# Performance work log

Measured on AMD Instinct MI355X. Metric: run time of the kernel, lower is better.

The kernel has to match this reference:

```python
import jax, jax.numpy as jnp
import numpy as np
from jax import lax

B, L = 16384, 32
HID, CIN = 8, 2
N_SUB = 2            # RK4 substeps per spline interval (fixed-step stand-in for torchcde's adaptive solver)
T10_LO, T10_HI = 0.1, 7.0


def push_zeros(a):
    # torch: move nonzero entries of each row to the right end, zeros to the left.
    # stable ascending sort on validity key (0 for zeros, 1 for valid) reproduces this exactly
    # because the invalid entries are exactly 0.
    keys = (a != 0).astype(jnp.int32)
    order = jnp.argsort(keys, axis=1)  # jax sorts are stable
    return jnp.take_along_axis(a, order, axis=1)


def setup_inputs() -> dict:
    key = jax.random.key(0)
    ks = jax.random.split(key, 12)
    fa_len = jax.random.randint(ks[0], (B, 1), L // 2, L + 1)          # 16..32 valid points
    valid = jnp.arange(L)[None, :] < fa_len                             # (B, L)
    X_fa_in = jnp.where(valid, jax.random.uniform(ks[1], (B, L), minval=0.1, maxval=1.1), 0.0)
    fa_vals_in = jnp.where(valid, jax.random.uniform(ks[2], (B, L), minval=0.05, maxval=0.45), 0.0)
    TR_vals = jax.random.uniform(ks[3], (B, 1), minval=0.003, maxval=0.01)
    fa_mask = valid

    def lin(k, fout, fin):
        kw, kb = jax.random.split(k)
        s = 1.0 / np.sqrt(fin)
        return (jax.random.uniform(kw, (fout, fin), minval=-s, maxval=s),
                jax.random.uniform(kb, (fout,), minval=-s, maxval=s))

    W_init, b_init = lin(ks[4], HID, CIN)        # self.initial: Linear(2, 8)
    W1, b1 = lin(ks[5], 256, HID)                # CDE_Func.linear1
    W2, b2 = lin(ks[6], CIN * HID, 256)          # CDE_Func.linear2
    Wr1, br1 = lin(ks[7], 200, HID)              # reg_T10
    Wr2, br2 = lin(ks[8], 200, 200)
    Wr3, br3 = lin(ks[9], 1, 200)
    return dict(X_fa_in=X_fa_in, fa_vals_in=fa_vals_in, TR_vals=TR_vals,
                W_init=W_init, b_init=b_init, W1=W1, b1=b1, W2=W2, b2=b2,
                Wr1=Wr1, br1=br1, Wr2=Wr2, br2=br2, Wr3=Wr3, br3=br3,
                fa_mask=fa_mask, fa_len=fa_len)


def _forward(X_fa_in, fa_vals_in, TR_vals, W_init, b_init, W1, b1, W2, b2,
             Wr1, br1, Wr2, br2, Wr3, br3, fa_mask, fa_len):
    fl = fa_len[:, 0]                       # (B,) int
    fl_f = fl.astype(X_fa_in.dtype)
    mean = jnp.sum(X_fa_in, axis=1) / fl_f
    Xn = X_fa_in / mean[:, None]
    X_fa = push_zeros(Xn)
    fa_vals = push_zeros(fa_vals_in)
    bidx = jnp.arange(X_fa.shape[0])
    last_X = X_fa[bidx, fl - 1][:, None]            # pushed array indexed at fa_len-1 (as in torch)
    last_fa = fa_vals_in[bidx, fl - 1][:, None]     # original array indexed at fa_len-1
    X_fa = jnp.where(X_fa == 0.0, last_X, X_fa)
    fa_vals = jnp.where(fa_vals == 0.0, last_fa, fa_vals)
    x = jnp.stack([fa_vals, X_fa], axis=-1)         # (B, L, 2): channels (fa, X)

    # Hermite cubic with backward differences, unit knot spacing t_i = i
    diffs = x[:, 1:] - x[:, :-1]                    # (B, L-1, C)
    m = jnp.concatenate([diffs[:, :1], diffs], axis=1)  # m_0 = fwd diff, m_i = backward diff
    X0s, X1s = x[:, :-1], x[:, 1:]                  # per-interval knot values (B, L-1, C)
    M0s, M1s = m[:, :-1], m[:, 1:]

    z0 = x[:, 0] @ W_init.T + b_init                # X.evaluate(interval[0]) == first knot

    def f(z):  # CDE vector field: (B, HID) -> (B, HID, CIN)
        h = jax.nn.relu(z @ W1.T + b1)
        g = jnp.tanh(h @ W2.T + b2)
        return g.reshape(z.shape[0], HID, CIN)

    hstep = 1.0 / N_SUB
    nI = x.shape[1] - 1
    intervals = jnp.repeat(jnp.arange(nI), N_SUB)
    s0s = jnp.tile(jnp.arange(N_SUB) * hstep, nI).astype(x.dtype)

    def step(z, ts):
        i, s0 = ts
        x0, x1 = X0s[:, i], X1s[:, i]
        m0, m1 = M0s[:, i], M1s[:, i]

        def dX(s):  # spline derivative dX/dt at local coord s in [0,1]
            s2 = s * s
            return ((6 * s2 - 6 * s) * x0 + (3 * s2 - 4 * s + 1) * m0 +
                    (-6 * s2 + 6 * s) * x1 + (3 * s2 - 2 * s) * m1)

        def F(s, zz):
            return jnp.einsum('bhc,bc->bh', f(zz), dX(s))

        k1 = F(s0, z)
        k2 = F(s0 + hstep / 2, z + 0.5 * hstep * k1)
        k3 = F(s0 + hstep / 2, z + 0.5 * hstep * k2)
        k4 = F(s0 + hstep, z + hstep * k3)
        return z + (hstep / 6) * (k1 + 2 * k2 + 2 * k3 + k4), None

    z_T, _ = lax.scan(step, z0, (intervals, s0s))

    h1 = jax.nn.gelu(z_T @ Wr1.T + br1, approximate=False)
    h2 = jax.nn.gelu(h1 @ Wr2.T + br2, approximate=False)
    t = (h2 @ Wr3.T + br3)[:, 0]
    T10 = T10_LO + jax.nn.sigmoid(t)[:, None] * (T10_HI - T10_LO)   # (B, 1)
    R1 = 1.0 / T10
    E = jnp.exp(-TR_vals * R1)                                      # (B, 1)
    X_out = (1 - E) * jnp.sin(fa_vals_in) / (1 - jnp.cos(fa_vals_in) * E)
    mean2 = jnp.sum(X_out, axis=1) / fl_f
    X_out = X_out / mean2[:, None]
    M0 = jnp.ones_like(T10)
    return X_out, T10, M0


def reference(X_fa_in, fa_vals_in, TR_vals, W_init, b_init, W1, b1, W2, b2,
              Wr1, br1, Wr2, br2, Wr3, br3, fa_mask, fa_len):
    return _forward(X_fa_in, fa_vals_in, TR_vals, W_init, b_init, W1, b1, W2, b2,
                    Wr1, br1, Wr2, br2, Wr3, br3, fa_mask, fa_len)
```

## Files before the change

kernel.cpp:

```cpp
#include <hip/hip_runtime.h>
#include <hip/hip_bf16.h>

#define B_ROWS 16384
#define L_SEQ  32

typedef _Float16 f16;
typedef __attribute__((ext_vector_type(8))) _Float16 f16x8;
typedef __attribute__((ext_vector_type(4))) float f32x4;
typedef __attribute__((ext_vector_type(4))) unsigned int u32x4;

__device__ __forceinline__ unsigned pkh(float a, float b) {
    return __builtin_bit_cast(unsigned, __builtin_amdgcn_cvt_pkrtz(a, b));
}
__device__ __forceinline__ float tanh_fast(float x) {
    float e = __expf(2.0f * x);
    float r = __builtin_amdgcn_rcpf(e + 1.0f);
    return fmaf(-2.0f, r, 1.0f);
}
__device__ __forceinline__ float gelu_exact(float x) {
    return 0.5f * x * (1.0f + erff(x * 0.70710678118654752440f));
}
__device__ __forceinline__ void pin4(u32x4& v) {
    unsigned x0 = v[0], x1 = v[1], x2 = v[2], x3 = v[3];
    asm volatile("" : "+v"(x0), "+v"(x1), "+v"(x2), "+v"(x3));
    v = (u32x4){x0, x1, x2, x3};
}

#define W2S_STRIDE 232
__global__ __launch_bounds__(256, 1) void fused_kernel(
    const float* __restrict__ Xin, const float* __restrict__ Fin,
    const float* __restrict__ TRv,
    const int*   __restrict__ fa_len,
    const float* __restrict__ Wi,  const float* __restrict__ bi,
    const float* __restrict__ W1g, const float* __restrict__ b1g,
    const float* __restrict__ W2g, const float* __restrict__ b2g,
    const float* __restrict__ Wr1, const float* __restrict__ br1,
    const float* __restrict__ Wr2, const float* __restrict__ br2,
    const float* __restrict__ Wr3, const float* __restrict__ br3,
    float* __restrict__ out)
{
    __shared__ __align__(16) float xm[64 * 132];
    __shared__ __align__(16) unsigned short w2s[208 * W2S_STRIDE];
#define XM(r_, i_, c_) xm[(r_) * 132 + (i_) * 4 + (c_)]

    const int tid = threadIdx.x;
    const int g16 = tid >> 4, sub = tid & 15;

    {
        const float4* src = (const float4*)Wr2;
#pragma unroll 4
        for (int v = tid; v < 10000; v += 256) {
            int row = v / 50, c = (v - row * 50) * 4;
            float4 w = src[v];
            *(uint2*)(&w2s[row * W2S_STRIDE + c]) =
                make_uint2(pkh(w.x, w.y), pkh(w.z, w.w));
        }
        for (int idx = tid; idx < 8 * W2S_STRIDE; idx += 256)
            w2s[200 * W2S_STRIDE + idx] = 0;
        for (int idx = tid; idx < 200 * 24; idx += 256) {
            int row = idx / 24, c = 200 + (idx - row * 24);
            w2s[row * W2S_STRIDE + c] = 0;
        }
    }

    float mean_r[4]; int fl_r[4];
#pragma unroll
    for (int r = 0; r < 4; ++r) {
        const int row_l = g16 * 4 + r;
        const int row   = blockIdx.x * 64 + row_l;
        const float* Xr = Xin + row * L_SEQ;
        const float* Fr = Fin + row * L_SEQ;
        float xr0 = Xr[sub], xr1 = Xr[sub + 16];
        float fr0 = Fr[sub], fr1 = Fr[sub + 16];
        fl_r[r] = fa_len[row];
        float s = xr0 + xr1;
        s += __shfl_xor(s, 1, 16);
        s += __shfl_xor(s, 2, 16);
        s += __shfl_xor(s, 4, 16);
        s += __shfl_xor(s, 8, 16);
        mean_r[r] = s / (float)fl_r[r];
        XM(row_l, sub, 0)      = fr0; XM(row_l, sub, 1)      = xr0;
        XM(row_l, sub + 16, 0) = fr1; XM(row_l, sub + 16, 1) = xr1;
    }
    __syncthreads();

    float ff[4][2], xf[4][2];
#pragma unroll
    for (int r = 0; r < 4; ++r) {
        const int row_l = g16 * 4 + r;
        const int fl = fl_r[r];
        const float mean = mean_r[r];
        const int shift = L_SEQ - fl;
        int lsrc  = fl - 1 - shift;
        int lsrcC = lsrc < 0 ? 0 : lsrc;
        float lastX = (lsrc >= 0) ? (XM(row_l, lsrcC, 1) / mean) : 0.0f;
        float lastF = XM(row_l, fl - 1, 0);
#pragma unroll
        for (int u = 0; u < 2; ++u) {
            int p = sub + u * 16;
            int src = p - shift;
            int sc  = src < 0 ? 0 : src;
            float fraw = XM(row_l, sc, 0);
            float xraw = XM(row_l, sc, 1);
            ff[r][u] = (src >= 0) ? fraw : lastF;
            xf[r][u] = (src >= 0) ? (xraw / mean) : lastX;
        }
    }
    __syncthreads();
#pragma unroll
    for (int r = 0; r < 4; ++r) {
        const int row_l = g16 * 4 + r;
#pragma unroll
        for (int u = 0; u < 2; ++u) {
            int p = sub + u * 16;
            XM(row_l, p, 0) = ff[r][u];
            XM(row_l, p, 1) = xf[r][u];
        }
    }
    __syncthreads();
#pragma unroll
    for (int r = 0; r < 4; ++r) {
        const int row_l = g16 * 4 + r;
#pragma unroll
        for (int u = 0; u < 2; ++u) {
            int p = sub + u * 16;
            int qd = (p == 0) ? 1 : p;
            XM(row_l, p, 2) = XM(row_l, qd, 0) - XM(row_l, qd - 1, 0);
            XM(row_l, p, 3) = XM(row_l, qd, 1) - XM(row_l, qd - 1, 1);
        }
    }
    __syncthreads();

    const int wv   = tid >> 6;
    const int lane = tid & 63;
    const int n    = lane & 15;
    const int q    = lane >> 4;
    const int rowl = wv * 16 + n;
    const int rowg = blockIdx.x * 64 + rowl;

    u32x4 a1[16];
#pragma unroll
    for (int t = 0; t < 16; ++t) {
        const float* wr = W1g + (t * 16 + n) * 8 + (q < 2 ? q * 4 : 0);
        float4 w4 = *(const float4*)wr;
        float b1v = b1g[t * 16 + n];
        unsigned d0 = (q < 2) ? pkh(w4.x, w4.y) : (q == 2 ? pkh(b1v, 0.0f) : 0u);
        unsigned d1 = (q < 2) ? pkh(w4.z, w4.w) : 0u;
        a1[t] = (u32x4){d0, d1, 0u, 0u};
        pin4(a1[t]);
    }
    u32x4 a2[8];
#pragma unroll
    for (int kk = 0; kk < 8; ++kk) {
        const float* w2r = W2g + n * 256 + kk * 32 + 4 * q;
        float4 p0 = *(const float4*)(w2r);
        float4 p1 = *(const float4*)(w2r + 16);
        a2[kk] = (u32x4){pkh(p0.x, p0.y), pkh(p0.z, p0.w), pkh(p1.x, p1.y), pkh(p1.z, p1.w)};
        pin4(a2[kk]);
    }
    f32x4 c2seed;
#pragma unroll
    for (int r = 0; r < 4; ++r) c2seed[r] = b2g[4 * q + r];

    float f0 = XM(rowl, 0, 0), X0 = XM(rowl, 0, 1);
    float z0 = fmaf(Wi[(2 * q) * 2], f0, fmaf(Wi[(2 * q) * 2 + 1], X0, bi[2 * q]));
    float z1 = fmaf(Wi[(2 * q + 1) * 2], f0, fmaf(Wi[(2 * q + 1) * 2 + 1], X0, bi[2 * q + 1]));

    const int bpi = (((q & 1) << 5) + n) << 2;
    const f32x4 zero4 = {0.f, 0.f, 0.f, 0.f};
    const f16x8 zf16 = {0, 0, 0, 0, 0, 0, 0, 0};

    auto make_bz = [&](float zza, float zzb) -> f16x8 {
        unsigned myz = pkh(zza, zzb);
        int b0 = __builtin_amdgcn_ds_bpermute(bpi, (int)myz);
        int b1 = __builtin_amdgcn_ds_bpermute(bpi + 64, (int)myz);
        unsigned bz0 = (q < 2) ? (unsigned)b0 : (q == 2 ? 0x3C00u : 0u);
        unsigned bz1 = (q < 2) ? (unsigned)b1 : 0u;
        return __builtin_bit_cast(f16x8, (u32x4){bz0, bz1, 0u, 0u});
    };

    auto FEVAL = [&](float zza, float zzb, float d0c, float d1c, float& ko0, float& ko1) {
        f16x8 bz = make_bz(zza, zzb);

        f32x4 c1[16];
#pragma unroll
        for (int t = 0; t < 16; ++t)
            c1[t] = __builtin_amdgcn_mfma_f32_16x16x32_f16(
                __builtin_bit_cast(f16x8, a1[t]), bz, zero4, 0, 0, 0);

        f16x8 hf[8];
#pragma unroll
        for (int kk = 0; kk < 8; ++kk) {
            u32x4 w = (u32x4){pkh(c1[2 * kk][0],     c1[2 * kk][1]),
                              pkh(c1[2 * kk][2],     c1[2 * kk][3]),
                              pkh(c1[2 * kk + 1][0], c1[2 * kk + 1][1]),
                              pkh(c1[2 * kk + 1][2], c1[2 * kk + 1][3])};
            hf[kk] = __builtin_elementwise_max(__builtin_bit_cast(f16x8, w), zf16);
        }

        f32x4 c2a = c2seed, c2b = zero4;
#pragma unroll
        for (int kk = 0; kk < 4; ++kk) {
            c2a = __builtin_amdgcn_mfma_f32_16x16x32_f16(
                __builtin_bit_cast(f16x8, a2[kk]), hf[kk], c2a, 0, 0, 0);
            c2b = __builtin_amdgcn_mfma_f32_16x16x32_f16(
                __builtin_bit_cast(f16x8, a2[kk + 4]), hf[kk + 4], c2b, 0, 0, 0);
        }
        f32x4 G = c2a + c2b;

        float t0 = tanh_fast(G[0]), t1 = tanh_fast(G[1]);
        float t2 = tanh_fast(G[2]), t3 = tanh_fast(G[3]);
        ko0 = fmaf(t0, d0c, t1 * d1c);
        ko1 = fmaf(t2, d0c, t3 * d1c);
    };

#pragma unroll 1
    for (int i = 0; i < 31; ++i) {
        float4 P0 = *(const float4*)&XM(rowl, i, 0);
        float4 P1 = *(const float4*)&XM(rowl, i + 1, 0);
        float m0f = P0.z, m0X = P0.w, m1f = P1.z, m1X = P1.w;
        float df  = P0.x - P1.x, dXx = P0.y - P1.y;

        float d25f = fmaf(-1.125f, df,  fmaf(0.1875f, m0f, -0.3125f * m1f));
        float d25X = fmaf(-1.125f, dXx, fmaf(0.1875f, m0X, -0.3125f * m1X));
        float d50f = fmaf(-1.5f,   df,  fmaf(-0.25f,  m0f, -0.25f   * m1f));
        float d50X = fmaf(-1.5f,   dXx, fmaf(-0.25f,  m0X, -0.25f   * m1X));
        float d75f = fmaf(-1.125f, df,  fmaf(-0.3125f, m0f, 0.1875f * m1f));
        float d75X = fmaf(-1.125f, dXx, fmaf(-0.3125f, m0X, 0.1875f * m1X));

#pragma unroll 1
        for (int ssi = 0; ssi < 2; ++ssi) {
            float daf = ssi ? d50f : m0f,  daX = ssi ? d50X : m0X;
            float dbf = ssi ? d75f : d25f, dbX = ssi ? d75X : d25X;
            float ddf = ssi ? m1f  : d50f, ddX = ssi ? m1X  : d50X;

            float k1a, k1b, k2a, k2b, k3a, k3b, k4a, k4b, zza, zzb;
            FEVAL(z0, z1, daf, daX, k1a, k1b);
            zza = fmaf(0.25f, k1a, z0); zzb = fmaf(0.25f, k1b, z1);
            FEVAL(zza, zzb, dbf, dbX, k2a, k2b);
            zza = fmaf(0.25f, k2a, z0); zzb = fmaf(0.25f, k2b, z1);
            FEVAL(zza, zzb, dbf, dbX, k3a, k3b);
            zza = fmaf(0.5f, k3a, z0);  zzb = fmaf(0.5f, k3b, z1);
            FEVAL(zza, zzb, ddf, ddX, k4a, k4b);

            float ka = fmaf(2.f, k2a, k1a); ka = fmaf(2.f, k3a, ka);
            float kb = fmaf(2.f, k2b, k1b); kb = fmaf(2.f, k3b, kb);
            z0 = fmaf(1.f / 12.f, ka + k4a, z0);
            z1 = fmaf(1.f / 12.f, kb + k4b, z1);
        }
    }

    f16x8 bz = make_bz(z0, z1);
    f32x4 c1r[13];
#pragma unroll
    for (int t = 0; t < 13; ++t) {
        int m = 16 * t + n;
        u32x4 af = {0u, 0u, 0u, 0u};
        if (q < 2) {
            if (m < 200) {
                float4 w4 = *(const float4*)(Wr1 + m * 8 + 4 * q);
                af[0] = pkh(w4.x, w4.y);
                af[1] = pkh(w4.z, w4.w);
            }
        } else if (q == 2) {
            float b = (m < 200) ? br1[m] : 0.0f;
            af[0] = pkh(b, 0.0f);
        }
        c1r[t] = __builtin_amdgcn_mfma_f32_16x16x32_f16(
            __builtin_bit_cast(f16x8, af), bz, zero4, 0, 0, 0);
    }

    f16x8 hf2[7];
#pragma unroll
    for (int kk = 0; kk < 7; ++kk) {
        float g0 = gelu_exact(c1r[2 * kk][0]), g1 = gelu_exact(c1r[2 * kk][1]);
        float g2 = gelu_exact(c1r[2 * kk][2]), g3 = gelu_exact(c1r[2 * kk][3]);
        float g4 = 0.f, g5 = 0.f, g6 = 0.f, g7 = 0.f;
        if (kk < 6) {
            g4 = gelu_exact(c1r[2 * kk + 1][0]); g5 = gelu_exact(c1r[2 * kk + 1][1]);
            g6 = gelu_exact(c1r[2 * kk + 1][2]); g7 = gelu_exact(c1r[2 * kk + 1][3]);
        }
        u32x4 w = (u32x4){pkh(g0, g1), pkh(g2, g3), pkh(g4, g5), pkh(g6, g7)};
        hf2[kk] = __builtin_bit_cast(f16x8, w);
    }

    float tpart = 0.0f;
#pragma unroll 1
    for (int mt = 0; mt < 13; ++mt) {
        int mb = 16 * mt + 4 * q;
        f32x4 c2 = zero4;
        if (mb + 3 < 200) c2 = *(const f32x4*)(br2 + mb);
        const unsigned short* ap = &w2s[(16 * mt + n) * W2S_STRIDE + 4 * q];
#pragma unroll
        for (int kk = 0; kk < 7; ++kk) {
            uint2 lo = *(const uint2*)(ap + 32 * kk);
            uint2 hi = *(const uint2*)(ap + 32 * kk + 16);
            u32x4 af = {lo.x, lo.y, hi.x, hi.y};
            c2 = __builtin_amdgcn_mfma_f32_16x16x32_f16(
                __builtin_bit_cast(f16x8, af), hf2[kk], c2, 0, 0, 0);
        }
        float4 w3 = make_float4(0.f, 0.f, 0.f, 0.f);
        if (mb + 3 < 200) w3 = *(const float4*)(Wr3 + mb);
        tpart = fmaf(w3.x, gelu_exact(c2[0]), tpart);
        tpart = fmaf(w3.y, gelu_exact(c2[1]), tpart);
        tpart = fmaf(w3.z, gelu_exact(c2[2]), tpart);
        tpart = fmaf(w3.w, gelu_exact(c2[3]), tpart);
    }
    tpart += __shfl_xor(tpart, 16);
    tpart += __shfl_xor(tpart, 32);

    float tval = tpart + br3[0];
    float sig  = __fdividef(1.0f, 1.0f + __expf(-tval));
    float T10  = 0.1f + 6.9f * sig;
    float E    = __expf(-TRv[rowg] * __builtin_amdgcn_rcpf(T10));

    const float* Fr = Fin + rowg * 32 + 8 * q;
    float xo[8]; float ssum = 0.0f;
#pragma unroll
    for (int j = 0; j < 8; ++j) {
        float fa = Fr[j];
        float sn = __sinf(fa), cs = __cosf(fa);
        float v = __fdividef((1.0f - E) * sn, 1.0f - cs * E);
        xo[j] = v; ssum += v;
    }
    ssum += __shfl_xor(ssum, 16);
    ssum += __shfl_xor(ssum, 32);
    float mean2 = ssum / (float)fa_len[rowg];
    float inv   = __fdividef(1.0f, mean2);

    float4* dst = (float4*)(out + rowg * 32 + 8 * q);
    dst[0] = make_float4(xo[0] * inv, xo[1] * inv, xo[2] * inv, xo[3] * inv);
    dst[1] = make_float4(xo[4] * inv, xo[5] * inv, xo[6] * inv, xo[7] * inv);
    if (q == 0) {
        out[B_ROWS * L_SEQ + rowg] = T10;
        out[B_ROWS * L_SEQ + B_ROWS + rowg] = 1.0f;
    }
#undef XM
}

extern "C" void kernel_launch(void* const* d_in, const int* in_sizes, int n_in,
                              void* d_out, int out_size, void* d_ws, size_t ws_size,
                              hipStream_t stream) {
    const float* Xin  = (const float*)d_in[0];
    const float* Fin  = (const float*)d_in[1];
    const float* TRv  = (const float*)d_in[2];
    const float* Wi   = (const float*)d_in[3];
    const float* bi   = (const float*)d_in[4];
    const float* W1g  = (const float*)d_in[5];
    const float* b1g  = (const float*)d_in[6];
    const float* W2g  = (const float*)d_in[7];
    const float* b2g  = (const float*)d_in[8];
    const float* Wr1  = (const float*)d_in[9];
    const float* br1  = (const float*)d_in[10];
    const float* Wr2  = (const float*)d_in[11];
    const float* br2  = (const float*)d_in[12];
    const float* Wr3  = (const float*)d_in[13];
    const float* br3  = (const float*)d_in[14];
    const int*   flen = (const int*)d_in[16];

    float* outp = (float*)d_out;
    (void)d_ws; (void)ws_size;

    fused_kernel<<<dim3(B_ROWS / 64), dim3(256), 0, stream>>>(
        Xin, Fin, TRv, flen, Wi, bi, W1g, b1g, W2g, b2g,
        Wr1, br1, Wr2, br2, Wr3, br3, outp);
}
```

Measured before the change: 251.7 us.

## Halve rows per block, drop LDS Wr2 staging, use 16x16x16 MFMA

Each block now handles 32 rows instead of 64, so each 16-lane MFMA column group covers only 8 distinct rows with duplicated lanes. The grid doubles to 1024 blocks and launch bounds allow 2 blocks per CU. The shared-memory copy of Wr2 in fp16 is removed, and the regression head now reads Wr2 from global memory with on-the-fly packing. The first-layer MFMAs switch to the K=16 variant with smaller operand registers. The intent is higher occupancy and less LDS setup per block, at the cost of half-wasted MFMA columns, duplicated ODE work, and repeated global reads and conversions of Wr2.

```diff
diff --git a/kernel.cpp b/kernel.cpp
--- a/kernel.cpp
+++ b/kernel.cpp
@@ -5,6 +5,7 @@
 #define L_SEQ  32
 
 typedef _Float16 f16;
+typedef __attribute__((ext_vector_type(4))) _Float16 f16x4;
 typedef __attribute__((ext_vector_type(8))) _Float16 f16x8;
 typedef __attribute__((ext_vector_type(4))) float f32x4;
 typedef __attribute__((ext_vector_type(4))) unsigned int u32x4;
@@ -20,14 +21,18 @@
 __device__ __forceinline__ float gelu_exact(float x) {
     return 0.5f * x * (1.0f + erff(x * 0.70710678118654752440f));
 }
+__device__ __forceinline__ void pin2(uint2& v) {
+    unsigned x0 = v.x, x1 = v.y;
+    asm volatile("" : "+v"(x0), "+v"(x1));
+    v = make_uint2(x0, x1);
+}
 __device__ __forceinline__ void pin4(u32x4& v) {
     unsigned x0 = v[0], x1 = v[1], x2 = v[2], x3 = v[3];
     asm volatile("" : "+v"(x0), "+v"(x1), "+v"(x2), "+v"(x3));
     v = (u32x4){x0, x1, x2, x3};
 }
 
-#define W2S_STRIDE 232
-__global__ __launch_bounds__(256, 1) void fused_kernel(
+__global__ __launch_bounds__(256, 2) void fused_kernel(
     const float* __restrict__ Xin, const float* __restrict__ Fin,
     const float* __restrict__ TRv,
     const int*   __restrict__ fa_len,
@@ -39,35 +44,17 @@
     const float* __restrict__ Wr3, const float* __restrict__ br3,
     float* __restrict__ out)
 {
-    __shared__ __align__(16) float xm[64 * 132];
-    __shared__ __align__(16) unsigned short w2s[208 * W2S_STRIDE];
+    __shared__ __align__(16) float xm[32 * 132];
 #define XM(r_, i_, c_) xm[(r_) * 132 + (i_) * 4 + (c_)]
 
     const int tid = threadIdx.x;
     const int g16 = tid >> 4, sub = tid & 15;
 
-    {
-        const float4* src = (const float4*)Wr2;
-#pragma unroll 4
-        for (int v = tid; v < 10000; v += 256) {
-            int row = v / 50, c = (v - row * 50) * 4;
-            float4 w = src[v];
-            *(uint2*)(&w2s[row * W2S_STRIDE + c]) =
-                make_uint2(pkh(w.x, w.y), pkh(w.z, w.w));
-        }
-        for (int idx = tid; idx < 8 * W2S_STRIDE; idx += 256)
-            w2s[200 * W2S_STRIDE + idx] = 0;
-        for (int idx = tid; idx < 200 * 24; idx += 256) {
-            int row = idx / 24, c = 200 + (idx - row * 24);
-            w2s[row * W2S_STRIDE + c] = 0;
-        }
-    }
-
-    float mean_r[4]; int fl_r[4];
-#pragma unroll
-    for (int r = 0; r < 4; ++r) {
-        const int row_l = g16 * 4 + r;
-        const int row   = blockIdx.x * 64 + row_l;
+    float mean_r[2]; int fl_r[2];
+#pragma unroll
+    for (int r = 0; r < 2; ++r) {
+        const int row_l = g16 * 2 + r;
+        const int row   = blockIdx.x * 32 + row_l;
         const float* Xr = Xin + row * L_SEQ;
         const float* Fr = Fin + row * L_SEQ;
         float xr0 = Xr[sub], xr1 = Xr[sub + 16];
@@ -84,10 +71,10 @@
     }
     __syncthreads();
 
-    float ff[4][2], xf[4][2];
-#pragma unroll
-    for (int r = 0; r < 4; ++r) {
-        const int row_l = g16 * 4 + r;
+    float ff[2][2], xf[2][2];
+#pragma unroll
+    for (int r = 0; r < 2; ++r) {
+        const int row_l = g16 * 2 + r;
         const int fl = fl_r[r];
         const float mean = mean_r[r];
         const int shift = L_SEQ - fl;
@@ -108,8 +95,8 @@
     }
     __syncthreads();
 #pragma unroll
-    for (int r = 0; r < 4; ++r) {
-        const int row_l = g16 * 4 + r;
+    for (int r = 0; r < 2; ++r) {
+        const int row_l = g16 * 2 + r;
 #pragma unroll
         for (int u = 0; u < 2; ++u) {
             int p = sub + u * 16;
@@ -119,8 +106,8 @@
     }
     __syncthreads();
 #pragma unroll
-    for (int r = 0; r < 4; ++r) {
-        const int row_l = g16 * 4 + r;
+    for (int r = 0; r < 2; ++r) {
+        const int row_l = g16 * 2 + r;
 #pragma unroll
         for (int u = 0; u < 2; ++u) {
             int p = sub + u * 16;
@@ -135,10 +122,11 @@
     const int lane = tid & 63;
     const int n    = lane & 15;
     const int q    = lane >> 4;
-    const int rowl = wv * 16 + n;
-    const int rowg = blockIdx.x * 64 + rowl;
-
-    u32x4 a1[16];
+    const int nr   = n & 7;
+    const int rowl = wv * 8 + nr;
+    const int rowg = blockIdx.x * 32 + rowl;
+
+    uint2 a1[16];
 #pragma unroll
     for (int t = 0; t < 16; ++t) {
         const float* wr = W1g + (t * 16 + n) * 8 + (q < 2 ? q * 4 : 0);
@@ -146,8 +134,8 @@
         float b1v = b1g[t * 16 + n];
         unsigned d0 = (q < 2) ? pkh(w4.x, w4.y) : (q == 2 ? pkh(b1v, 0.0f) : 0u);
         unsigned d1 = (q < 2) ? pkh(w4.z, w4.w) : 0u;
-        a1[t] = (u32x4){d0, d1, 0u, 0u};
-        pin4(a1[t]);
+        a1[t] = make_uint2(d0, d1);
+        pin2(a1[t]);
     }
     u32x4 a2[8];
 #pragma unroll
@@ -170,23 +158,24 @@
     const f32x4 zero4 = {0.f, 0.f, 0.f, 0.f};
     const f16x8 zf16 = {0, 0, 0, 0, 0, 0, 0, 0};
 
-    auto make_bz = [&](float zza, float zzb) -> f16x8 {
+    auto make_bz = [&](float zza, float zzb) -> uint2 {
         unsigned myz = pkh(zza, zzb);
         int b0 = __builtin_amdgcn_ds_bpermute(bpi, (int)myz);
         int b1 = __builtin_amdgcn_ds_bpermute(bpi + 64, (int)myz);
         unsigned bz0 = (q < 2) ? (unsigned)b0 : (q == 2 ? 0x3C00u : 0u);
         unsigned bz1 = (q < 2) ? (unsigned)b1 : 0u;
-        return __builtin_bit_cast(f16x8, (u32x4){bz0, bz1, 0u, 0u});
+        return make_uint2(bz0, bz1);
     };
 
     auto FEVAL = [&](float zza, float zzb, float d0c, float d1c, float& ko0, float& ko1) {
-        f16x8 bz = make_bz(zza, zzb);
+        uint2 bzp = make_bz(zza, zzb);
+        f16x4 bz = __builtin_bit_cast(f16x4, bzp);
 
         f32x4 c1[16];
 #pragma unroll
         for (int t = 0; t < 16; ++t)
-            c1[t] = __builtin_amdgcn_mfma_f32_16x16x32_f16(
-                __builtin_bit_cast(f16x8, a1[t]), bz, zero4, 0, 0, 0);
+            c1[t] = __builtin_amdgcn_mfma_f32_16x16x16f16(
+                __builtin_bit_cast(f16x4, a1[t]), bz, zero4, 0, 0, 0);
 
         f16x8 hf[8];
 #pragma unroll
@@ -250,24 +239,24 @@
         }
     }
 
-    f16x8 bz = make_bz(z0, z1);
+    uint2 bzp = make_bz(z0, z1);
+    f16x4 bzr = __builtin_bit_cast(f16x4, bzp);
     f32x4 c1r[13];
 #pragma unroll
     for (int t = 0; t < 13; ++t) {
         int m = 16 * t + n;
-        u32x4 af = {0u, 0u, 0u, 0u};
+        uint2 afp = make_uint2(0u, 0u);
         if (q < 2) {
             if (m < 200) {
                 float4 w4 = *(const float4*)(Wr1 + m * 8 + 4 * q);
-                af[0] = pkh(w4.x, w4.y);
-                af[1] = pkh(w4.z, w4.w);
+                afp = make_uint2(pkh(w4.x, w4.y), pkh(w4.z, w4.w));
             }
         } else if (q == 2) {
             float b = (m < 200) ? br1[m] : 0.0f;
-            af[0] = pkh(b, 0.0f);
-        }
-        c1r[t] = __builtin_amdgcn_mfma_f32_16x16x32_f16(
-            __builtin_bit_cast(f16x8, af), bz, zero4, 0, 0, 0);
+            afp.x = pkh(b, 0.0f);
+        }
+        c1r[t] = __builtin_amdgcn_mfma_f32_16x16x16f16(
+            __builtin_bit_cast(f16x4, afp), bzr, zero4, 0, 0, 0);
     }
 
     f16x8 hf2[7];
@@ -290,12 +279,22 @@
         int mb = 16 * mt + 4 * q;
         f32x4 c2 = zero4;
         if (mb + 3 < 200) c2 = *(const f32x4*)(br2 + mb);
-        const unsigned short* ap = &w2s[(16 * mt + n) * W2S_STRIDE + 4 * q];
+        int m2 = 16 * mt + n;
 #pragma unroll
         for (int kk = 0; kk < 7; ++kk) {
-            uint2 lo = *(const uint2*)(ap + 32 * kk);
-            uint2 hi = *(const uint2*)(ap + 32 * kk + 16);
-            u32x4 af = {lo.x, lo.y, hi.x, hi.y};
+            u32x4 af = {0u, 0u, 0u, 0u};
+            if (m2 < 200) {
+                int k0 = 32 * kk + 4 * q;
+                const float* wr = Wr2 + m2 * 200 + k0;
+                if (k0 + 3 < 200) {
+                    float4 wa = *(const float4*)(wr);
+                    af[0] = pkh(wa.x, wa.y); af[1] = pkh(wa.z, wa.w);
+                }
+                if (k0 + 19 < 200) {
+                    float4 wb = *(const float4*)(wr + 16);
+                    af[2] = pkh(wb.x, wb.y); af[3] = pkh(wb.z, wb.w);
+                }
+            }
             c2 = __builtin_amdgcn_mfma_f32_16x16x32_f16(
                 __builtin_bit_cast(f16x8, af), hf2[kk], c2, 0, 0, 0);
         }
@@ -328,12 +327,14 @@
     float mean2 = ssum / (float)fa_len[rowg];
     float inv   = __fdividef(1.0f, mean2);
 
-    float4* dst = (float4*)(out + rowg * 32 + 8 * q);
-    dst[0] = make_float4(xo[0] * inv, xo[1] * inv, xo[2] * inv, xo[3] * inv);
-    dst[1] = make_float4(xo[4] * inv, xo[5] * inv, xo[6] * inv, xo[7] * inv);
-    if (q == 0) {
-        out[B_ROWS * L_SEQ + rowg] = T10;
-        out[B_ROWS * L_SEQ + B_ROWS + rowg] = 1.0f;
+    if (n < 8) {
+        float4* dst = (float4*)(out + rowg * 32 + 8 * q);
+        dst[0] = make_float4(xo[0] * inv, xo[1] * inv, xo[2] * inv, xo[3] * inv);
+        dst[1] = make_float4(xo[4] * inv, xo[5] * inv, xo[6] * inv, xo[7] * inv);
+        if (q == 0) {
+            out[B_ROWS * L_SEQ + rowg] = T10;
+            out[B_ROWS * L_SEQ + B_ROWS + rowg] = 1.0f;
+        }
     }
 #undef XM
 }
@@ -361,7 +362,7 @@
     float* outp = (float*)d_out;
     (void)d_ws; (void)ws_size;
 
-    fused_kernel<<<dim3(B_ROWS / 64), dim3(256), 0, stream>>>(
+    fused_kernel<<<dim3(B_ROWS / 32), dim3(256), 0, stream>>>(
         Xin, Fin, TRv, flen, Wi, bi, W1g, b1g, W2g, b2g,
         Wr1, br1, Wr2, br2, Wr3, br3, outp);
 }
```

After: 279.7 us. 11.1% more time.
